# Performance work log

Hardware: AMD Instinct MI355X
Metric: run time of the kernel (lower is better)

The kernel has to match this reference:

```python
import jax, jax.numpy as jnp
import numpy as np

HIDDEN = 512
LATENT = 256
BATCH = 1024
SEQ_LEN = 256


def setup_inputs() -> dict:
    key = jax.random.key(0)
    ks = jax.random.split(key, 12)
    s_h = 1.0 / np.sqrt(2 * HIDDEN)
    s_c = 1.0 / np.sqrt(LATENT)
    return {
        "h": jax.random.normal(ks[0], (BATCH, HIDDEN), jnp.float32),
        "c": jax.random.normal(ks[1], (BATCH, HIDDEN), jnp.float32),
        "seq_len": SEQ_LEN,
        # init-state projections: Linear(2*hidden, latent)
        "init_h_W": jax.random.uniform(ks[2], (LATENT, 2 * HIDDEN), jnp.float32, -s_h, s_h),
        "init_h_b": jax.random.uniform(ks[3], (LATENT,), jnp.float32, -s_h, s_h),
        "init_c_W": jax.random.uniform(ks[4], (LATENT, 2 * HIDDEN), jnp.float32, -s_h, s_h),
        "init_c_b": jax.random.uniform(ks[5], (LATENT,), jnp.float32, -s_h, s_h),
        # LSTM cell: input dim = hidden, state dim = latent, gates stacked [i, f, g, o]
        "W_ih": jax.random.uniform(ks[6], (4 * LATENT, HIDDEN), jnp.float32, -s_c, s_c),
        "W_hh": jax.random.uniform(ks[7], (4 * LATENT, LATENT), jnp.float32, -s_c, s_c),
        "b_ih": jax.random.uniform(ks[8], (4 * LATENT,), jnp.float32, -s_c, s_c),
        "b_hh": jax.random.uniform(ks[9], (4 * LATENT,), jnp.float32, -s_c, s_c),
    }


def reference(h, c, seq_len, init_h_W, init_h_b, init_c_W, init_c_b, W_ih, W_hh, b_ih, b_hh):
    # init states: ELU(Linear(cat(h, c)))
    hc = jnp.concatenate([h, c], axis=1)                     # [B, 2H]
    h_t = jax.nn.elu(hc @ init_h_W.T + init_h_b)             # [B, L]
    c_t = jax.nn.elu(hc @ init_c_W.T + init_c_b)             # [B, L]

    # input to the cell is the constant encoder state h -> precompute its projection once
    x_proj = h @ W_ih.T + b_ih + b_hh                        # [B, 4L]

    def step(carry, _):
        h_t, c_t = carry
        gates = x_proj + h_t @ W_hh.T                        # [B, 4L]
        i, f, g, o = jnp.split(gates, 4, axis=1)
        c_n = jax.nn.sigmoid(f) * c_t + jax.nn.sigmoid(i) * jnp.tanh(g)
        h_n = jax.nn.sigmoid(o) * jnp.tanh(c_n)
        return (h_n, c_n), h_n

    _, ys = jax.lax.scan(step, (h_t, c_t), None, length=seq_len)  # ys: [T, B, L]
    return jnp.transpose(ys, (1, 0, 2))                      # [B, T, L]
```

## Files before the change

kernel.cpp:

```cpp
#include <hip/hip_runtime.h>
#include <stdint.h>

typedef __attribute__((ext_vector_type(4))) float f32x4;
typedef __attribute__((ext_vector_type(8))) _Float16 f16x8;

static __device__ __forceinline__ unsigned short f2h(float f) {
    union { _Float16 h; unsigned short u; } v;
    v.h = (_Float16)f;
    return v.u;
}
static __device__ __forceinline__ f16x8 as_f16x8(uint4 v) {
    union { uint4 u; f16x8 s; } x; x.u = v; return x.s;
}
static __device__ __forceinline__ float sigmoid_fast(float x) {
    return __builtin_amdgcn_rcpf(1.0f + __builtin_amdgcn_exp2f(-1.4426950408889634f * x));
}
static __device__ __forceinline__ float tanh_fast(float x) {
    return 1.0f - 2.0f * __builtin_amdgcn_rcpf(1.0f + __builtin_amdgcn_exp2f(2.8853900817779268f * x));
}
static __device__ __forceinline__ void lds_barrier() {
    __builtin_amdgcn_s_waitcnt(0xc07f);
    __builtin_amdgcn_s_barrier();
}

__global__ __launch_bounds__(256) void convert_all(
    const float* __restrict__ h, const float* __restrict__ c,
    const float* __restrict__ iWh, const float* __restrict__ iWc,
    const float* __restrict__ Wih, const float* __restrict__ Whh,
    unsigned short* __restrict__ hc_h, unsigned short* __restrict__ iWh_h,
    unsigned short* __restrict__ iWc_h, unsigned short* __restrict__ Wih_h,
    unsigned short* __restrict__ Whh_h) {
    int i = blockIdx.x * 256 + threadIdx.x;
    const float* src; unsigned short* dst;
    if (i < 131072) {
        int base = i * 4, r = base >> 9, cc = base & 511;
        src = h + base; dst = hc_h + r * 1024 + cc;
    } else if (i < 262144) {
        int j = i - 131072; int base = j * 4, r = base >> 9, cc = base & 511;
        src = c + base; dst = hc_h + r * 1024 + 512 + cc;
    } else if (i < 327680) { int j = i - 262144; src = iWh + j * 4; dst = iWh_h + j * 4; }
    else if (i < 393216)   { int j = i - 327680; src = iWc + j * 4; dst = iWc_h + j * 4; }
    else if (i < 524288)   { int j = i - 393216; src = Wih + j * 4; dst = Wih_h + j * 4; }
    else                   { int j = i - 524288; src = Whh + j * 4; dst = Whh_h + j * 4; }
    float4 v = *(const float4*)src;
    dst[0] = f2h(v.x); dst[1] = f2h(v.y); dst[2] = f2h(v.z); dst[3] = f2h(v.w);
}

__global__ __launch_bounds__(256) void gemm_bt(
    const unsigned short* __restrict__ A, const unsigned short* __restrict__ W,
    float* __restrict__ C, const float* __restrict__ b1, const float* __restrict__ b2,
    int K, int lda, int ldw, int N, int do_elu, int bias_row) {
    __shared__ unsigned short As[64][40];
    __shared__ unsigned short Bs[64][40];
    int tid = threadIdx.x;
    int lane = tid & 63, wv = tid >> 6;
    int q = lane >> 4, l15 = lane & 15;
    int Mbase = blockIdx.x * 64, Nbase = blockIdx.y * 64;
    int ldrow = tid >> 2, seg = tid & 3;
    const unsigned short* Ap = A + (size_t)(Mbase + ldrow) * lda + seg * 8;
    const unsigned short* Wp = W + (size_t)(Nbase + ldrow) * ldw + seg * 8;
    f32x4 acc[4] = {};
    for (int k0 = 0; k0 < K; k0 += 32) {
        uint4 av = *(const uint4*)(Ap + k0);
        uint4 wvv = *(const uint4*)(Wp + k0);
        __syncthreads();
        *(uint4*)(&As[ldrow][seg * 8]) = av;
        *(uint4*)(&Bs[ldrow][seg * 8]) = wvv;
        __syncthreads();
        f16x8 af = *(const f16x8*)(&As[wv * 16 + l15][q * 8]);
#pragma unroll
        for (int nt = 0; nt < 4; nt++) {
            f16x8 bf = *(const f16x8*)(&Bs[nt * 16 + l15][q * 8]);
            acc[nt] = __builtin_amdgcn_mfma_f32_16x16x32_f16(af, bf, acc[nt], 0, 0, 0);
        }
    }
#pragma unroll
    for (int nt = 0; nt < 4; nt++) {
        int col = Nbase + nt * 16 + l15;
        float bcol = bias_row ? 0.0f : (b1[col] + (b2 ? b2[col] : 0.0f));
#pragma unroll
        for (int r = 0; r < 4; r++) {
            int row = Mbase + wv * 16 + q * 4 + r;
            float bias = bias_row ? (b1[row] + (b2 ? b2[row] : 0.0f)) : bcol;
            float v = acc[nt][r] + bias;
            if (do_elu) v = v > 0.0f ? v : (__builtin_amdgcn_exp2f(1.4426950408889634f * v) - 1.0f);
            C[(size_t)row * N + col] = v;
        }
    }
}

__global__ __launch_bounds__(256) void gemm_init(
    const unsigned short* __restrict__ A,
    const unsigned short* __restrict__ W0, const unsigned short* __restrict__ W1,
    float* __restrict__ C0, float* __restrict__ C1,
    const float* __restrict__ bias0, const float* __restrict__ bias1) {
    const unsigned short* W = blockIdx.z ? W1 : W0;
    float* C = blockIdx.z ? C1 : C0;
    const float* bias = blockIdx.z ? bias1 : bias0;
    __shared__ unsigned short As[64][40];
    __shared__ unsigned short Bs[64][40];
    int tid = threadIdx.x;
    int lane = tid & 63, wv = tid >> 6;
    int q = lane >> 4, l15 = lane & 15;
    int Mbase = blockIdx.x * 64, Nbase = blockIdx.y * 64;
    int ldrow = tid >> 2, seg = tid & 3;
    const unsigned short* Ap = A + (size_t)(Mbase + ldrow) * 1024 + seg * 8;
    const unsigned short* Wp = W + (size_t)(Nbase + ldrow) * 1024 + seg * 8;
    f32x4 acc[4] = {};
    for (int k0 = 0; k0 < 1024; k0 += 32) {
        uint4 av = *(const uint4*)(Ap + k0);
        uint4 wvv = *(const uint4*)(Wp + k0);
        __syncthreads();
        *(uint4*)(&As[ldrow][seg * 8]) = av;
        *(uint4*)(&Bs[ldrow][seg * 8]) = wvv;
        __syncthreads();
        f16x8 af = *(const f16x8*)(&As[wv * 16 + l15][q * 8]);
#pragma unroll
        for (int nt = 0; nt < 4; nt++) {
            f16x8 bf = *(const f16x8*)(&Bs[nt * 16 + l15][q * 8]);
            acc[nt] = __builtin_amdgcn_mfma_f32_16x16x32_f16(af, bf, acc[nt], 0, 0, 0);
        }
    }
#pragma unroll
    for (int nt = 0; nt < 4; nt++) {
        int col = Nbase + nt * 16 + l15;
        float b = bias[col];
#pragma unroll
        for (int r = 0; r < 4; r++) {
            int row = Mbase + wv * 16 + q * 4 + r;
            float v = acc[nt][r] + b;
            v = v > 0.0f ? v : (__builtin_amdgcn_exp2f(1.4426950408889634f * v) - 1.0f);
            C[(size_t)row * 256 + col] = v;
        }
    }
}

#define HB_STRIDE 264
#define HB_HALF   (16 * HB_STRIDE)
#define WLDS_OFF  (2 * HB_HALF * 2)
#define WFRAGS    17
#define LSTM_LDS_BYTES (WLDS_OFF + 8 * WFRAGS * 1024)

__global__ __launch_bounds__(512, 2) void lstm_rec(
    const unsigned short* __restrict__ Whh,
    const float* __restrict__ xpT,
    const float* __restrict__ h0,
    const float* __restrict__ c0,
    const int* __restrict__ seq_len,
    float* __restrict__ out)
{
    __shared__ uint4 smem4[LSTM_LDS_BYTES / 16];
    unsigned short* hbuf = (unsigned short*)smem4;
    unsigned char* wlds = (unsigned char*)smem4 + WLDS_OFF;
    const int tid = threadIdx.x;
    const int lane = tid & 63, wv = tid >> 6;
    const int q = lane >> 4, l15 = lane & 15;
    const int T = *seq_len;
    const int rowbase = blockIdx.x * 16;

    {
        int e = tid * 8;
        int r = e >> 8, cc = e & 255;
        const float* s = h0 + (size_t)(rowbase + r) * 256 + cc;
        float4 v0 = *(const float4*)s;
        float4 v1 = *(const float4*)(s + 4);
        unsigned short* d = hbuf + r * HB_STRIDE + cc;
        d[0] = f2h(v0.x); d[1] = f2h(v0.y); d[2] = f2h(v0.z); d[3] = f2h(v0.w);
        d[4] = f2h(v1.x); d[5] = f2h(v1.y); d[6] = f2h(v1.z); d[7] = f2h(v1.w);
    }

    const unsigned short* wb = Whh + wv * 8192 + l15 * 256 + q * 8;

    uint4 wreg[47];
#pragma unroll
    for (int kt = 0; kt < 6; kt++)
#pragma unroll
        for (int g = 0; g < 4; g++)
#pragma unroll
            for (int ct = 0; ct < 2; ct++) {
                int fi = kt * 8 + g * 2 + ct;
                if (fi < 47)
                    wreg[fi] = *(const uint4*)(wb + (size_t)g * 65536 + ct * 4096 + kt * 32);
            }

    unsigned char* wlp = wlds + wv * (WFRAGS * 1024) + lane * 16;
#pragma unroll
    for (int fi = 0; fi < WFRAGS; fi++) {
        int kt = (fi < 8) ? 6 : (fi < 16 ? 7 : 5);
        int p  = (fi < 16) ? (fi & 7) : 7;
        int g = p >> 1, ct = p & 1;
        uint4 v = *(const uint4*)(wb + (size_t)g * 65536 + ct * 4096 + kt * 32);
        *(uint4*)(wlp + fi * 1024) = v;
    }

    float creg[8];
#pragma unroll
    for (int ct = 0; ct < 2; ct++)
#pragma unroll
        for (int r = 0; r < 4; r++)
            creg[ct * 4 + r] = c0[(size_t)(rowbase + q * 4 + r) * 256 + wv * 32 + ct * 16 + l15];

    const float* xpb = xpT + (size_t)(wv * 32 + l15) * 1024 + rowbase + (q << 2);
    f32x4 acc[8];
#pragma unroll
    for (int p = 0; p < 8; p++)
        acc[p] = *(const f32x4*)(xpb + (size_t)(p >> 1) * 262144 + (p & 1) * 16384);

    float* outp = out + ((size_t)(rowbase + q * 4) * T) * 256 + wv * 32 + l15;

    __syncthreads();

    for (int t = 0; t < T; t++) {
        const unsigned short* hb = hbuf + (t & 1) * HB_HALF + l15 * HB_STRIDE + q * 8;
#pragma unroll
        for (int kt = 0; kt < 8; kt++) {
            f16x8 af = *(const f16x8*)(hb + kt * 32);
#pragma unroll
            for (int p = 0; p < 8; p++) {
                f16x8 bf;
                if (kt < 6 && !(kt == 5 && p == 7))
                    bf = as_f16x8(wreg[kt * 8 + p]);
                else if (kt == 6)
                    bf = *(const f16x8*)(wlp + p * 1024);
                else if (kt == 7)
                    bf = *(const f16x8*)(wlp + (8 + p) * 1024);
                else
                    bf = *(const f16x8*)(wlp + 16 * 1024);
                acc[p] = __builtin_amdgcn_mfma_f32_16x16x32_f16(af, bf, acc[p], 0, 0, 0);
            }
        }
        float hv[8];
#pragma unroll
        for (int ct = 0; ct < 2; ct++)
#pragma unroll
            for (int r = 0; r < 4; r++) {
                float ig = sigmoid_fast(acc[0 + ct][r]);
                float fg = sigmoid_fast(acc[2 + ct][r]);
                float gg = tanh_fast(acc[4 + ct][r]);
                float og = sigmoid_fast(acc[6 + ct][r]);
                float cn = fg * creg[ct * 4 + r] + ig * gg;
                creg[ct * 4 + r] = cn;
                hv[ct * 4 + r] = og * tanh_fast(cn);
            }
#pragma unroll
        for (int p = 0; p < 8; p++)
            acc[p] = *(const f32x4*)(xpb + (size_t)(p >> 1) * 262144 + (p & 1) * 16384);
        __builtin_amdgcn_sched_barrier(0);
        unsigned short* hn = hbuf + ((t + 1) & 1) * HB_HALF + (q * 4) * HB_STRIDE + wv * 32 + l15;
#pragma unroll
        for (int ct = 0; ct < 2; ct++)
#pragma unroll
            for (int r = 0; r < 4; r++) {
                hn[r * HB_STRIDE + ct * 16] = f2h(hv[ct * 4 + r]);
                outp[(size_t)r * T * 256 + ct * 16] = hv[ct * 4 + r];
            }
        outp += 256;
        lds_barrier();
    }
}

extern "C" void kernel_launch(void* const* d_in, const int* in_sizes, int n_in,
                              void* d_out, int out_size, void* d_ws, size_t ws_size,
                              hipStream_t stream) {
    const float* h   = (const float*)d_in[0];
    const float* c   = (const float*)d_in[1];
    const int*   seqp= (const int*)d_in[2];
    const float* iWh = (const float*)d_in[3];
    const float* ibh = (const float*)d_in[4];
    const float* iWc = (const float*)d_in[5];
    const float* ibc = (const float*)d_in[6];
    const float* Wih = (const float*)d_in[7];
    const float* Whh = (const float*)d_in[8];
    const float* bih = (const float*)d_in[9];
    const float* bhh = (const float*)d_in[10];
    float* out = (float*)d_out;
    unsigned char* ws = (unsigned char*)d_ws;

    unsigned short* hc_h  = (unsigned short*)(ws + 0);
    unsigned short* iWh_h = (unsigned short*)(ws + 2097152);
    unsigned short* iWc_h = (unsigned short*)(ws + 2621440);
    unsigned short* Wih_h = (unsigned short*)(ws + 3145728);
    unsigned short* Whh_h = (unsigned short*)(ws + 4194304);
    float* h0  = (float*)(ws + 4718592);
    float* c0  = (float*)(ws + 5767168);
    float* xpT = (float*)(ws + 6815744);

    convert_all<<<2304, 256, 0, stream>>>(h, c, iWh, iWc, Wih, Whh,
                                          hc_h, iWh_h, iWc_h, Wih_h, Whh_h);

    gemm_init<<<dim3(16, 4, 2), 256, 0, stream>>>(hc_h, iWh_h, iWc_h, h0, c0, ibh, ibc);
    gemm_bt<<<dim3(16, 16), 256, 0, stream>>>(Wih_h, hc_h, xpT, bih, bhh,
                                              512, 512, 1024, 1024, 0, 1);

    lstm_rec<<<64, 512, 0, stream>>>(Whh_h, xpT, h0, c0, seqp, out);
}
```

Measured before the change: 1.298 ms.

## Hand-schedule recurrent MFMA loop with interleaved LDS weight prefetch

Moves one more W_hh fragment into registers (48 instead of 47) and shrinks the LDS weight area to the two k-tiles 6 and 7. The k loop is unrolled by hand so register-resident k-tiles are interleaved with LDS-resident ones. LDS B fragments are double-buffered in four registers and prefetched while other MFMAs run, hiding LDS latency inside the serial per-step chain. The h stores to LDS are also grouped before the global output stores. The cost is more register pressure, which could spill under launch_bounds(512,2).

```diff
diff --git a/kernel.cpp b/kernel.cpp
--- a/kernel.cpp
+++ b/kernel.cpp
@@ -138,7 +138,7 @@
 #define HB_STRIDE 264
 #define HB_HALF   (16 * HB_STRIDE)
 #define WLDS_OFF  (2 * HB_HALF * 2)
-#define WFRAGS    17
+#define WFRAGS    16
 #define LSTM_LDS_BYTES (WLDS_OFF + 8 * WFRAGS * 1024)
 
 __global__ __launch_bounds__(512, 2) void lstm_rec(
@@ -171,25 +171,18 @@
 
     const unsigned short* wb = Whh + wv * 8192 + l15 * 256 + q * 8;
 
-    uint4 wreg[47];
+    uint4 wreg[48];
 #pragma unroll
     for (int kt = 0; kt < 6; kt++)
 #pragma unroll
-        for (int g = 0; g < 4; g++)
-#pragma unroll
-            for (int ct = 0; ct < 2; ct++) {
-                int fi = kt * 8 + g * 2 + ct;
-                if (fi < 47)
-                    wreg[fi] = *(const uint4*)(wb + (size_t)g * 65536 + ct * 4096 + kt * 32);
-            }
+        for (int p = 0; p < 8; p++)
+            wreg[kt * 8 + p] = *(const uint4*)(wb + (size_t)(p >> 1) * 65536 + (p & 1) * 4096 + kt * 32);
 
     unsigned char* wlp = wlds + wv * (WFRAGS * 1024) + lane * 16;
 #pragma unroll
     for (int fi = 0; fi < WFRAGS; fi++) {
-        int kt = (fi < 8) ? 6 : (fi < 16 ? 7 : 5);
-        int p  = (fi < 16) ? (fi & 7) : 7;
-        int g = p >> 1, ct = p & 1;
-        uint4 v = *(const uint4*)(wb + (size_t)g * 65536 + ct * 4096 + kt * 32);
+        int kt = 6 + (fi >> 3), p = fi & 7;
+        uint4 v = *(const uint4*)(wb + (size_t)(p >> 1) * 65536 + (p & 1) * 4096 + kt * 32);
         *(uint4*)(wlp + fi * 1024) = v;
     }
 
@@ -208,27 +201,62 @@
 
     float* outp = out + ((size_t)(rowbase + q * 4) * T) * 256 + wv * 32 + l15;
 
+    uint4 lw[4];
+#pragma unroll
+    for (int j = 0; j < 4; j++) lw[j] = *(const uint4*)(wlp + j * 1024);
+
     __syncthreads();
 
     for (int t = 0; t < T; t++) {
         const unsigned short* hb = hbuf + (t & 1) * HB_HALF + l15 * HB_STRIDE + q * 8;
-#pragma unroll
-        for (int kt = 0; kt < 8; kt++) {
-            f16x8 af = *(const f16x8*)(hb + kt * 32);
-#pragma unroll
-            for (int p = 0; p < 8; p++) {
-                f16x8 bf;
-                if (kt < 6 && !(kt == 5 && p == 7))
-                    bf = as_f16x8(wreg[kt * 8 + p]);
-                else if (kt == 6)
-                    bf = *(const f16x8*)(wlp + p * 1024);
-                else if (kt == 7)
-                    bf = *(const f16x8*)(wlp + (8 + p) * 1024);
-                else
-                    bf = *(const f16x8*)(wlp + 16 * 1024);
-                acc[p] = __builtin_amdgcn_mfma_f32_16x16x32_f16(af, bf, acc[p], 0, 0, 0);
-            }
-        }
+        f16x8 afA, afB;
+        afA = *(const f16x8*)(hb + 0 * 32);
+        afB = *(const f16x8*)(hb + 1 * 32);
+#pragma unroll
+        for (int p = 0; p < 8; p++)
+            acc[p] = __builtin_amdgcn_mfma_f32_16x16x32_f16(afA, as_f16x8(wreg[0 * 8 + p]), acc[p], 0, 0, 0);
+        afA = *(const f16x8*)(hb + 6 * 32);
+#pragma unroll
+        for (int p = 0; p < 8; p++)
+            acc[p] = __builtin_amdgcn_mfma_f32_16x16x32_f16(afB, as_f16x8(wreg[1 * 8 + p]), acc[p], 0, 0, 0);
+        afB = *(const f16x8*)(hb + 2 * 32);
+#pragma unroll
+        for (int j = 0; j < 4; j++)
+            acc[j] = __builtin_amdgcn_mfma_f32_16x16x32_f16(afA, as_f16x8(lw[j]), acc[j], 0, 0, 0);
+#pragma unroll
+        for (int j = 0; j < 4; j++) lw[j] = *(const uint4*)(wlp + (4 + j) * 1024);
+#pragma unroll
+        for (int p = 0; p < 8; p++)
+            acc[p] = __builtin_amdgcn_mfma_f32_16x16x32_f16(afB, as_f16x8(wreg[2 * 8 + p]), acc[p], 0, 0, 0);
+        afB = *(const f16x8*)(hb + 3 * 32);
+#pragma unroll
+        for (int j = 0; j < 4; j++)
+            acc[4 + j] = __builtin_amdgcn_mfma_f32_16x16x32_f16(afA, as_f16x8(lw[j]), acc[4 + j], 0, 0, 0);
+#pragma unroll
+        for (int j = 0; j < 4; j++) lw[j] = *(const uint4*)(wlp + (8 + j) * 1024);
+        afA = *(const f16x8*)(hb + 7 * 32);
+#pragma unroll
+        for (int p = 0; p < 8; p++)
+            acc[p] = __builtin_amdgcn_mfma_f32_16x16x32_f16(afB, as_f16x8(wreg[3 * 8 + p]), acc[p], 0, 0, 0);
+        afB = *(const f16x8*)(hb + 4 * 32);
+#pragma unroll
+        for (int j = 0; j < 4; j++)
+            acc[j] = __builtin_amdgcn_mfma_f32_16x16x32_f16(afA, as_f16x8(lw[j]), acc[j], 0, 0, 0);
+#pragma unroll
+        for (int j = 0; j < 4; j++) lw[j] = *(const uint4*)(wlp + (12 + j) * 1024);
+#pragma unroll
+        for (int p = 0; p < 8; p++)
+            acc[p] = __builtin_amdgcn_mfma_f32_16x16x32_f16(afB, as_f16x8(wreg[4 * 8 + p]), acc[p], 0, 0, 0);
+        afB = *(const f16x8*)(hb + 5 * 32);
+#pragma unroll
+        for (int j = 0; j < 4; j++)
+            acc[4 + j] = __builtin_amdgcn_mfma_f32_16x16x32_f16(afA, as_f16x8(lw[j]), acc[4 + j], 0, 0, 0);
+#pragma unroll
+        for (int j = 0; j < 4; j++) lw[j] = *(const uint4*)(wlp + j * 1024);
+#pragma unroll
+        for (int p = 0; p < 8; p++)
+            acc[p] = __builtin_amdgcn_mfma_f32_16x16x32_f16(afB, as_f16x8(wreg[5 * 8 + p]), acc[p], 0, 0, 0);
+
         float hv[8];
 #pragma unroll
         for (int ct = 0; ct < 2; ct++)
@@ -250,10 +278,13 @@
 #pragma unroll
         for (int ct = 0; ct < 2; ct++)
 #pragma unroll
-            for (int r = 0; r < 4; r++) {
+            for (int r = 0; r < 4; r++)
                 hn[r * HB_STRIDE + ct * 16] = f2h(hv[ct * 4 + r]);
+#pragma unroll
+        for (int ct = 0; ct < 2; ct++)
+#pragma unroll
+            for (int r = 0; r < 4; r++)
                 outp[(size_t)r * T * 256 + ct * 16] = hv[ct * 4 + r];
-            }
         outp += 256;
         lds_barrier();
     }
```

After: 1.269 ms. 2.3% less time.
